# Kernel tuning notes

Measured on AMD Instinct MI355X. Metric: run time of the kernel, lower is better.

The kernel has to match this reference:

```python
import jax, jax.numpy as jnp
import numpy as np
from jax import lax

B, C, H, W = 4, 192, 64, 64
D_STATE, D_CONV, EXPAND = 16, 4, 2
D_INNER = EXPAND * C           # 384
DT_RANK = (C + 15) // 16       # 12 (mamba_ssm default ceil(d_model/16))


def setup_inputs() -> dict:
    key = jax.random.key(0)
    ks = jax.random.split(key, 12)
    sc = lambda k, shape, s=0.02: (jax.random.normal(k, shape, jnp.float32) * s)
    x = jax.random.normal(ks[0], (B, C, H, W), jnp.float32)
    norm_w = jnp.ones((C,), jnp.float32)
    norm_b = jnp.zeros((C,), jnp.float32)
    in_proj_w = sc(ks[1], (2 * D_INNER, C))
    conv_w = sc(ks[2], (D_INNER, D_CONV), 0.1)
    conv_b = jnp.zeros((D_INNER,), jnp.float32)
    x_proj_w = sc(ks[3], (DT_RANK + 2 * D_STATE, D_INNER))
    dt_proj_w = sc(ks[4], (D_INNER, DT_RANK), 0.1)
    # dt bias init so softplus(dt_bias) is in a realistic [1e-3, 1e-1] range
    dt0 = jax.random.uniform(ks[5], (D_INNER,), jnp.float32, 0.001, 0.1)
    dt_proj_b = jnp.log(jnp.expm1(dt0))
    A_log = jnp.log(jnp.broadcast_to(
        jnp.arange(1, D_STATE + 1, dtype=jnp.float32), (D_INNER, D_STATE)))
    D = jnp.ones((D_INNER,), jnp.float32)
    out_proj_w = sc(ks[6], (C, D_INNER))
    return {"x": x, "norm_w": norm_w, "norm_b": norm_b, "in_proj_w": in_proj_w,
            "conv_w": conv_w, "conv_b": conv_b, "x_proj_w": x_proj_w,
            "dt_proj_w": dt_proj_w, "dt_proj_b": dt_proj_b, "A_log": A_log,
            "D": D, "out_proj_w": out_proj_w}


def _mamba2d(x, norm_w, norm_b, in_proj_w, conv_w, conv_b, x_proj_w,
             dt_proj_w, dt_proj_b, A_log, D, out_proj_w):
    b, c, h, w = x.shape
    L = h * w
    seq = x.reshape(b, c, L).transpose(0, 2, 1)            # (B, L, C)
    # LayerNorm over channel dim
    mu = seq.mean(-1, keepdims=True)
    var = ((seq - mu) ** 2).mean(-1, keepdims=True)
    seqn = (seq - mu) * lax.rsqrt(var + 1e-5) * norm_w + norm_b
    # in_proj -> (x, z)
    xz = seqn @ in_proj_w.T                                # (B, L, 2*d_inner)
    xin, z = jnp.split(xz, 2, axis=-1)
    # causal depthwise conv1d over L
    xc = xin.transpose(0, 2, 1)                            # (B, d_inner, L)
    xc = lax.conv_general_dilated(xc, conv_w[:, None, :], (1,),
                                  [(D_CONV - 1, 0)],
                                  feature_group_count=D_INNER)
    xc = jax.nn.silu(xc + conv_b[None, :, None])
    xs = xc.transpose(0, 2, 1)                             # (B, L, d_inner)
    # input-dependent dt, B, C
    dbl = xs @ x_proj_w.T                                  # (B, L, dt_rank+2n)
    dt = dbl[..., :DT_RANK]
    Bm = dbl[..., DT_RANK:DT_RANK + D_STATE]               # (B, L, n)
    Cm = dbl[..., DT_RANK + D_STATE:]                      # (B, L, n)
    dt = jax.nn.softplus(dt @ dt_proj_w.T + dt_proj_b)     # (B, L, d_inner)
    A = -jnp.exp(A_log)                                    # (d_inner, n)
    dA = jnp.exp(dt[..., None] * A)                        # (B, L, d_inner, n)
    dBx = jnp.einsum('bld,bln->bldn', dt * xs, Bm)         # (B, L, d_inner, n)
    # selective scan over L
    def step(hcar, inp):
        dA_t, dBx_t, C_t = inp
        hcar = dA_t * hcar + dBx_t                         # (B, d_inner, n)
        y_t = jnp.einsum('bdn,bn->bd', hcar, C_t)
        return hcar, y_t
    h0 = jnp.zeros((b, D_INNER, D_STATE), xs.dtype)
    _, ys = lax.scan(step, h0, (jnp.moveaxis(dA, 1, 0),
                                jnp.moveaxis(dBx, 1, 0),
                                jnp.moveaxis(Cm, 1, 0)))
    y = jnp.moveaxis(ys, 0, 1) + xs * D                    # (B, L, d_inner)
    y = y * jax.nn.silu(z)
    out = y @ out_proj_w.T                                 # (B, L, C)
    return x + out.transpose(0, 2, 1).reshape(b, c, h, w)


def reference(x, norm_w, norm_b, in_proj_w, conv_w, conv_b, x_proj_w,
              dt_proj_w, dt_proj_b, A_log, D, out_proj_w):
    return _mamba2d(x, norm_w, norm_b, in_proj_w, conv_w, conv_b, x_proj_w,
                    dt_proj_w, dt_proj_b, A_log, D, out_proj_w)
```

## Files before the change

### kernel.cpp

```cpp
#include <hip/hip_runtime.h>
#include <hip/hip_bf16.h>

constexpr int B_ = 4;
constexpr int C_ = 192;
constexpr int L_ = 4096;
constexpr int DI = 384;
constexpr int DSs = 16;
constexpr int DTR = 12;
constexpr int NDBL = 44;
constexpr int NCHUNK = 256;
constexpr int CSZ = 16;

constexpr size_t BL = (size_t)B_ * L_;

constexpr size_t F_SEQN = 0;
constexpr size_t F_XIN  = F_SEQN + BL * C_ / 2;
constexpr size_t F_Z    = F_XIN + BL * DI / 2;
constexpr size_t F_XSB  = F_Z + BL * DI / 2;
constexpr size_t F_DBL  = F_XSB + BL * DI / 2;
constexpr size_t F_DT   = F_DBL + BL * NDBL;
constexpr size_t F_SBUF = F_DT + BL * DI / 2;
constexpr size_t F_HLOC = F_SBUF + (size_t)B_ * NCHUNK * DI;
constexpr size_t F_WBUF = F_HLOC + (size_t)B_ * NCHUNK * DI * 16 / 2;

typedef __attribute__((ext_vector_type(8))) short bf16x8;
typedef __attribute__((ext_vector_type(4))) float f32x4;

__device__ __forceinline__ unsigned short f2bf(float v) {
  unsigned x = __builtin_bit_cast(unsigned, v);
  unsigned r = x + 0x7FFFu + ((x >> 16) & 1u);
  return (unsigned short)(r >> 16);
}
__device__ __forceinline__ float bf2f(unsigned short u) {
  return __builtin_bit_cast(float, (unsigned)u << 16);
}
__device__ __forceinline__ void gload16(const void* g, void* l) {
  __builtin_amdgcn_global_load_lds((const __attribute__((address_space(1))) void*)g,
                                   (__attribute__((address_space(3))) void*)l, 16, 0, 0);
}
#define MFMA16(a, b, c) __builtin_amdgcn_mfma_f32_16x16x32_bf16(a, b, c, 0, 0, 0)

__global__ __launch_bounds__(256) void k_ln(const float* __restrict__ x,
                                            const float* __restrict__ nw,
                                            const float* __restrict__ nb,
                                            unsigned short* __restrict__ seqn,
                                            const float* __restrict__ ipw,
                                            const float* __restrict__ xpw,
                                            const float* __restrict__ opw,
                                            unsigned short* __restrict__ wbuf) {
  if (blockIdx.x >= 256) {
    int t = (blockIdx.x - 256) * 256 + threadIdx.x;
    if (t < 239616) {
      float v;
      if (t < 147456) v = ipw[t];
      else if (t < 165888) {
        int j = t - 147456;
        int r = j / 384, c = j - r * 384;
        v = (r < 44) ? xpw[r * 384 + c] : 0.f;
      } else v = opw[t - 165888];
      wbuf[t] = f2bf(v);
    }
    return;
  }
  __shared__ unsigned short xt[192][66];
  __shared__ float ps[4][64], ps2[4][64];
  __shared__ float mu_[64], rs_[64];
  __shared__ float wsh[192], bsh[192];
  int tid = threadIdx.x;
  int blk = blockIdx.x;
  int b = blk >> 6;
  int l0 = (blk & 63) << 6;
  const float* xb = x + (size_t)b * C_ * L_;
  for (int idx = tid; idx < 192 * 16; idx += 256) {
    int c = idx >> 4, lq = idx & 15;
    float4 v = *(const float4*)&xb[(size_t)c * L_ + l0 + (lq << 2)];
    ushort2 u0, u1;
    u0.x = f2bf(v.x); u0.y = f2bf(v.y);
    u1.x = f2bf(v.z); u1.y = f2bf(v.w);
    *(ushort2*)&xt[c][(lq << 2)] = u0;
    *(ushort2*)&xt[c][(lq << 2) + 2] = u1;
  }
  if (tid < 192) { wsh[tid] = nw[tid]; bsh[tid] = nb[tid]; }
  __syncthreads();
  int ll = tid & 63, q = tid >> 6;
  float s = 0.f, ss = 0.f;
  for (int c = q * 48; c < q * 48 + 48; ++c) {
    float v = bf2f(xt[c][ll]);
    s += v; ss += v * v;
  }
  ps[q][ll] = s; ps2[q][ll] = ss;
  __syncthreads();
  if (q == 0) {
    float st = ps[0][ll] + ps[1][ll] + ps[2][ll] + ps[3][ll];
    float sst = ps2[0][ll] + ps2[1][ll] + ps2[2][ll] + ps2[3][ll];
    float mu = st * (1.f / 192.f);
    float var = sst * (1.f / 192.f) - mu * mu;
    mu_[ll] = mu; rs_[ll] = rsqrtf(var + 1e-5f);
  }
  __syncthreads();
  unsigned short* so = seqn + ((size_t)b * L_ + l0) * C_;
  for (int idx = tid; idx < 64 * 192; idx += 256) {
    int l = idx / 192, c = idx - l * 192;
    so[idx] = f2bf((bf2f(xt[c][l]) - mu_[l]) * rs_[l] * wsh[c] + bsh[c]);
  }
}

__global__ __launch_bounds__(256) void k_inproj(const unsigned short* __restrict__ A,
                                                const unsigned short* __restrict__ W,
                                                unsigned short* __restrict__ xin,
                                                unsigned short* __restrict__ z) {
  __shared__ unsigned short smem[16384];
  unsigned short* As = smem;
  unsigned short* Bs = smem + 8192;
  int tid = threadIdx.x;
  int w = tid >> 6, l = tid & 63;
  int wr = w >> 1, wc = w & 1;
  int m0 = blockIdx.x << 7;
  int n0 = blockIdx.y << 7;
  f32x4 acc[4][4];
#pragma unroll
  for (int i = 0; i < 4; ++i)
#pragma unroll
    for (int j = 0; j < 4; ++j) acc[i][j] = (f32x4){0.f, 0.f, 0.f, 0.f};
  int lr = l & 15, lk = l >> 4;
  for (int kt = 0; kt < 3; ++kt) {
    int k0 = kt * 64;
    if (kt) __syncthreads();
#pragma unroll
    for (int i = 0; i < 4; ++i) {
      int row = (i << 5) + (tid >> 3);
      int gc = k0 + (((tid & 7) ^ (row & 7)) << 3);
      gload16(A + (size_t)(m0 + row) * 192 + gc, &As[(i << 11) + (w << 9)]);
      gload16(W + (size_t)(n0 + row) * 192 + gc, &Bs[(i << 11) + (w << 9)]);
    }
    __syncthreads();
#pragma unroll
    for (int ks = 0; ks < 2; ++ks) {
      int s = (ks << 2) + lk;
      bf16x8 af[4], bfr[4];
#pragma unroll
      for (int mi = 0; mi < 4; ++mi) {
        int r = (wr << 6) + (mi << 4) + lr;
        af[mi] = *(const bf16x8*)&As[r * 64 + ((s ^ (r & 7)) << 3)];
      }
#pragma unroll
      for (int ni = 0; ni < 4; ++ni) {
        int r = (wc << 6) + (ni << 4) + lr;
        bfr[ni] = *(const bf16x8*)&Bs[r * 64 + ((s ^ (r & 7)) << 3)];
      }
#pragma unroll
      for (int mi = 0; mi < 4; ++mi)
#pragma unroll
        for (int ni = 0; ni < 4; ++ni) acc[mi][ni] = MFMA16(af[mi], bfr[ni], acc[mi][ni]);
    }
  }
  __syncthreads();
#pragma unroll
  for (int mi = 0; mi < 4; ++mi)
#pragma unroll
    for (int ni = 0; ni < 4; ++ni) {
      int col = (wc << 6) + (ni << 4) + lr;
#pragma unroll
      for (int r = 0; r < 4; ++r) {
        int row = (wr << 6) + (mi << 4) + (lk << 2) + r;
        smem[(row << 7) + col] = f2bf(acc[mi][ni][r]);
      }
    }
  __syncthreads();
#pragma unroll
  for (int i = 0; i < 8; ++i) {
    int chunk = i * 256 + tid;
    int row = chunk >> 4, cq = chunk & 15;
    int n = n0 + (cq << 3);
    unsigned short* dst = (n < 384) ? (xin + (size_t)(m0 + row) * DI + n)
                                    : (z + (size_t)(m0 + row) * DI + (n - 384));
    *(bf16x8*)dst = *(const bf16x8*)&smem[(row << 7) + (cq << 3)];
  }
}

__global__ __launch_bounds__(384) void k_convx(const unsigned short* __restrict__ xin,
                                               const float* __restrict__ cw,
                                               const float* __restrict__ cb,
                                               const unsigned short* __restrict__ W,
                                               unsigned short* __restrict__ xsb,
                                               float* __restrict__ dbl) {
  __shared__ unsigned short xs[6 * 4096];
  __shared__ unsigned short Bs[3072];
  int tid = threadIdx.x;
  int w = tid >> 6, l = tid & 63;
  int b = blockIdx.y;
  int l0 = blockIdx.x << 6;
  int d = tid;
  float4 w4 = *(const float4*)&cw[d * 4];
  float bb = cb[d];
  const unsigned short* xp = xin + ((size_t)b * L_ + l0) * DI + d;
  unsigned short* op = xsb + ((size_t)b * L_ + l0) * DI + d;
  float x0 = 0.f, x1 = 0.f, x2 = 0.f;
  if (l0 > 0) {
    x0 = bf2f(*(xp - 3 * DI));
    x1 = bf2f(*(xp - 2 * DI));
    x2 = bf2f(*(xp - DI));
  }
  int kt = d >> 6, col = d & 63, g = col >> 3, e = col & 7;
  unsigned short* xsrow = xs + kt * 4096;
  for (int r = 0; r < 64; ++r) {
    float xv = bf2f(xp[(size_t)r * DI]);
    float a = bb + w4.x * x0 + w4.y * x1 + w4.z * x2 + w4.w * xv;
    float sv = a * __builtin_amdgcn_rcpf(1.f + __expf(-a));
    unsigned short sb = f2bf(sv);
    xsrow[r * 64 + ((g ^ (r & 7)) << 3) + e] = sb;
    op[(size_t)r * DI] = sb;
    x0 = x1; x1 = x2; x2 = xv;
  }
  __syncthreads();
  int lr = l & 15, lk = l >> 4;
  f32x4 acc[3];
#pragma unroll
  for (int i = 0; i < 3; ++i) acc[i] = (f32x4){0.f, 0.f, 0.f, 0.f};
  for (int kt2 = 0; kt2 < 6; ++kt2) {
    int k0 = kt2 * 64;
    if (kt2) __syncthreads();
    {
      int row = tid >> 3;
      int gc = k0 + (((tid & 7) ^ (row & 7)) << 3);
      gload16(W + (size_t)row * 384 + gc, &Bs[w << 9]);
    }
    __syncthreads();
    if (w < 4) {
#pragma unroll
      for (int ks = 0; ks < 2; ++ks) {
        int s = (ks << 2) + lk;
        int ar = (w << 4) + lr;
        bf16x8 a = *(const bf16x8*)&xs[kt2 * 4096 + ar * 64 + ((s ^ (ar & 7)) << 3)];
#pragma unroll
        for (int ni = 0; ni < 3; ++ni) {
          int br = (ni << 4) + lr;
          bf16x8 bbv = *(const bf16x8*)&Bs[br * 64 + ((s ^ (br & 7)) << 3)];
          acc[ni] = MFMA16(a, bbv, acc[ni]);
        }
      }
    }
  }
  if (w < 4) {
#pragma unroll
    for (int ni = 0; ni < 3; ++ni)
#pragma unroll
      for (int r = 0; r < 4; ++r) {
        int colq = (ni << 4) + lr;
        if (colq < NDBL)
          dbl[((size_t)b * L_ + l0 + (w << 4) + (lk << 2) + r) * NDBL + colq] = acc[ni][r];
      }
  }
}

__global__ __launch_bounds__(384) void k_scanA(const unsigned short* __restrict__ xsb,
                                               const float* __restrict__ dbl,
                                               const float* __restrict__ dw,
                                               const float* __restrict__ dbias,
                                               const float* __restrict__ A_log,
                                               unsigned short* __restrict__ dtb,
                                               unsigned short* __restrict__ Hloc,
                                               float* __restrict__ Sbuf) {
  __shared__ float Bsh[CSZ][16];
  __shared__ float dl[CSZ][12];
  int tid = threadIdx.x;
  int blk = blockIdx.x;
  int b = blk >> 8;
  int chunk = blk & (NCHUNK - 1);
  int l0 = chunk * CSZ;
  for (int idx = tid; idx < CSZ * 28; idx += 384) {
    int r = idx / 28, c = idx - r * 28;
    float v = dbl[((size_t)b * L_ + l0 + r) * NDBL + c];
    if (c < 12) dl[r][c] = v; else Bsh[r][c - 12] = v;
  }
  int d = tid;
  float4 wv0 = *(const float4*)&dw[d * 12];
  float4 wv1 = *(const float4*)&dw[d * 12 + 4];
  float4 wv2 = *(const float4*)&dw[d * 12 + 8];
  float bias = dbias[d];
  bool fast = true;
#pragma unroll
  for (int n = 0; n < 16; ++n) {
    float An_ = -__expf(A_log[d * 16 + n]);
    fast = fast && (fabsf(An_ + (float)(n + 1)) < 2e-3f);
  }
  const unsigned short* xp = xsb + ((size_t)b * L_ + l0) * DI + d;
  unsigned short* dtp = dtb + ((size_t)b * L_ + l0) * DI + d;
  __syncthreads();
  float h[16];
#pragma unroll
  for (int n = 0; n < 16; ++n) h[n] = 0.f;
  float S = 0.f;
  if (fast) {
#pragma unroll
    for (int i = 0; i < CSZ; ++i) {
      float4 c0 = *(const float4*)&dl[i][0];
      float4 c1 = *(const float4*)&dl[i][4];
      float4 c2 = *(const float4*)&dl[i][8];
      float a = bias;
      a = fmaf(wv0.x, c0.x, a); a = fmaf(wv0.y, c0.y, a);
      a = fmaf(wv0.z, c0.z, a); a = fmaf(wv0.w, c0.w, a);
      a = fmaf(wv1.x, c1.x, a); a = fmaf(wv1.y, c1.y, a);
      a = fmaf(wv1.z, c1.z, a); a = fmaf(wv1.w, c1.w, a);
      a = fmaf(wv2.x, c2.x, a); a = fmaf(wv2.y, c2.y, a);
      a = fmaf(wv2.z, c2.z, a); a = fmaf(wv2.w, c2.w, a);
      float sp = fmaxf(a, 0.f) + __logf(1.f + __expf(-fabsf(a)));
      dtp[(size_t)i * DI] = f2bf(sp);
      S += sp;
      float xv = bf2f(xp[(size_t)i * DI]);
      float dtx = sp * xv;
      float r = __expf(-sp);
      float r2 = r * r;
      float r4 = r2 * r2;
      float dA0 = r, dA1 = r2, dA2 = r2 * r, dA3 = r4;
#pragma unroll
      for (int g = 0; g < 4; ++g) {
        float4 Bg = *(const float4*)&Bsh[i][g << 2];
        h[(g << 2) + 0] = fmaf(dA0, h[(g << 2) + 0], dtx * Bg.x);
        h[(g << 2) + 1] = fmaf(dA1, h[(g << 2) + 1], dtx * Bg.y);
        h[(g << 2) + 2] = fmaf(dA2, h[(g << 2) + 2], dtx * Bg.z);
        h[(g << 2) + 3] = fmaf(dA3, h[(g << 2) + 3], dtx * Bg.w);
        if (g < 3) { dA0 *= r4; dA1 *= r4; dA2 *= r4; dA3 *= r4; }
      }
    }
  } else {
    float An[16];
#pragma unroll
    for (int n = 0; n < 16; ++n) An[n] = -__expf(A_log[d * 16 + n]);
#pragma unroll
    for (int i = 0; i < CSZ; ++i) {
      float4 c0 = *(const float4*)&dl[i][0];
      float4 c1 = *(const float4*)&dl[i][4];
      float4 c2 = *(const float4*)&dl[i][8];
      float a = bias;
      a = fmaf(wv0.x, c0.x, a); a = fmaf(wv0.y, c0.y, a);
      a = fmaf(wv0.z, c0.z, a); a = fmaf(wv0.w, c0.w, a);
      a = fmaf(wv1.x, c1.x, a); a = fmaf(wv1.y, c1.y, a);
      a = fmaf(wv1.z, c1.z, a); a = fmaf(wv1.w, c1.w, a);
      a = fmaf(wv2.x, c2.x, a); a = fmaf(wv2.y, c2.y, a);
      a = fmaf(wv2.z, c2.z, a); a = fmaf(wv2.w, c2.w, a);
      float sp = fmaxf(a, 0.f) + __logf(1.f + __expf(-fabsf(a)));
      dtp[(size_t)i * DI] = f2bf(sp);
      S += sp;
      float xv = bf2f(xp[(size_t)i * DI]);
      float dtx = sp * xv;
#pragma unroll
      for (int n = 0; n < 16; ++n)
        h[n] = fmaf(__expf(sp * An[n]), h[n], dtx * Bsh[i][n]);
    }
  }
  size_t hbase = ((size_t)(b * NCHUNK + chunk) * 16) * DI + d;
#pragma unroll
  for (int n = 0; n < 16; ++n) Hloc[hbase + (size_t)n * DI] = f2bf(h[n]);
  Sbuf[((size_t)b * NCHUNK + chunk) * DI + d] = S;
}

__global__ __launch_bounds__(256) void k_scanB(const float* __restrict__ A_log,
                                               unsigned short* __restrict__ Hloc,
                                               const float* __restrict__ Sbuf) {
  int gid = blockIdx.x * 256 + threadIdx.x;
  int d = gid % DI;
  int rest = gid / DI;
  int n = rest & 15;
  int b = rest >> 4;
  float An = -__expf(A_log[d * 16 + n]);
  unsigned short* Hp = Hloc + ((size_t)b * NCHUNK * 16 + n) * DI + d;
  const float* Sp = Sbuf + (size_t)b * NCHUNK * DI + d;
  constexpr size_t HS = (size_t)16 * DI;
  float h = 0.f;
  float SA[8], HA[8], SB[8], HB[8];
#define LDGRP(Sa, Ha, cb)                         \
  _Pragma("unroll") for (int u = 0; u < 8; ++u) { \
    Sa[u] = Sp[(size_t)((cb) + u) * DI];          \
    Ha[u] = bf2f(Hp[(size_t)((cb) + u) * HS]);    \
  }
#define STGRP(Sa, Ha, cb)                         \
  _Pragma("unroll") for (int u = 0; u < 8; ++u) { \
    Hp[(size_t)((cb) + u) * HS] = f2bf(h);        \
    h = fmaf(__expf(An * Sa[u]), h, Ha[u]);       \
  }
  LDGRP(SA, HA, 0)
  for (int g = 0; g < 32; g += 2) {
    LDGRP(SB, HB, (g + 1) * 8)
    STGRP(SA, HA, g * 8)
    if (g + 2 < 32) LDGRP(SA, HA, (g + 2) * 8)
    STGRP(SB, HB, (g + 1) * 8)
  }
#undef LDGRP
#undef STGRP
}

__global__ __launch_bounds__(384) void k_scanC(const unsigned short* __restrict__ xsb,
                                               const unsigned short* __restrict__ dtb,
                                               const float* __restrict__ dbl,
                                               const unsigned short* __restrict__ z,
                                               const float* __restrict__ A_log,
                                               const float* __restrict__ Dw,
                                               const unsigned short* __restrict__ Hloc,
                                               unsigned short* __restrict__ ybuf) {
  __shared__ float BCsh[CSZ][32];
  int tid = threadIdx.x;
  int blk = blockIdx.x;
  int b = blk >> 8;
  int chunk = blk & (NCHUNK - 1);
  int l0 = chunk * CSZ;
  for (int idx = tid; idx < CSZ * 32; idx += 384) {
    int r = idx >> 5, n32 = idx & 31;
    BCsh[r][n32] = dbl[((size_t)b * L_ + l0 + r) * NDBL + DTR + n32];
  }
  int d = tid;
  float Dd = Dw[d];
  bool fast = true;
#pragma unroll
  for (int n = 0; n < 16; ++n) {
    float An_ = -__expf(A_log[d * 16 + n]);
    fast = fast && (fabsf(An_ + (float)(n + 1)) < 2e-3f);
  }
  size_t hbase = ((size_t)(b * NCHUNK + chunk) * 16) * DI + d;
  float h[16];
#pragma unroll
  for (int n = 0; n < 16; ++n) h[n] = bf2f(Hloc[hbase + (size_t)n * DI]);
  const unsigned short* xp = xsb + ((size_t)b * L_ + l0) * DI + d;
  const unsigned short* dtp = dtb + ((size_t)b * L_ + l0) * DI + d;
  const unsigned short* zp = z + ((size_t)b * L_ + l0) * DI + d;
  unsigned short* yp = ybuf + ((size_t)b * L_ + l0) * DI + d;
  __syncthreads();
  if (fast) {
#pragma unroll
    for (int i = 0; i < CSZ; ++i) {
      float sp = bf2f(dtp[(size_t)i * DI]);
      float xv = bf2f(xp[(size_t)i * DI]);
      float zv = bf2f(zp[(size_t)i * DI]);
      float dtx = sp * xv;
      float r = __expf(-sp);
      float r2 = r * r;
      float r4 = r2 * r2;
      float dA0 = r, dA1 = r2, dA2 = r2 * r, dA3 = r4;
      float y = 0.f;
#pragma unroll
      for (int g = 0; g < 4; ++g) {
        float4 Bg = *(const float4*)&BCsh[i][g << 2];
        float4 Cg = *(const float4*)&BCsh[i][16 + (g << 2)];
        h[(g << 2) + 0] = fmaf(dA0, h[(g << 2) + 0], dtx * Bg.x);
        h[(g << 2) + 1] = fmaf(dA1, h[(g << 2) + 1], dtx * Bg.y);
        h[(g << 2) + 2] = fmaf(dA2, h[(g << 2) + 2], dtx * Bg.z);
        h[(g << 2) + 3] = fmaf(dA3, h[(g << 2) + 3], dtx * Bg.w);
        y = fmaf(h[(g << 2) + 0], Cg.x, y);
        y = fmaf(h[(g << 2) + 1], Cg.y, y);
        y = fmaf(h[(g << 2) + 2], Cg.z, y);
        y = fmaf(h[(g << 2) + 3], Cg.w, y);
        if (g < 3) { dA0 *= r4; dA1 *= r4; dA2 *= r4; dA3 *= r4; }
      }
      y = fmaf(xv, Dd, y);
      float sig = __builtin_amdgcn_rcpf(1.f + __expf(-zv));
      yp[(size_t)i * DI] = f2bf(y * (zv * sig));
    }
  } else {
    float An[16];
#pragma unroll
    for (int n = 0; n < 16; ++n) An[n] = -__expf(A_log[d * 16 + n]);
#pragma unroll
    for (int i = 0; i < CSZ; ++i) {
      float sp = bf2f(dtp[(size_t)i * DI]);
      float xv = bf2f(xp[(size_t)i * DI]);
      float zv = bf2f(zp[(size_t)i * DI]);
      float dtx = sp * xv;
      float y = 0.f;
#pragma unroll
      for (int n = 0; n < 16; ++n) {
        h[n] = fmaf(__expf(sp * An[n]), h[n], dtx * BCsh[i][n]);
        y = fmaf(h[n], BCsh[i][16 + n], y);
      }
      y = fmaf(xv, Dd, y);
      float sig = __builtin_amdgcn_rcpf(1.f + __expf(-zv));
      yp[(size_t)i * DI] = f2bf(y * (zv * sig));
    }
  }
}

__global__ __launch_bounds__(256) void k_outproj(const unsigned short* __restrict__ Y,
                                                 const unsigned short* __restrict__ W,
                                                 const float* __restrict__ x,
                                                 float* __restrict__ out) {
  __shared__ float smemf[8448];
  unsigned short* As = (unsigned short*)smemf;
  unsigned short* Bs = (unsigned short*)smemf + 8192;
  int tid = threadIdx.x;
  int w = tid >> 6, l = tid & 63;
  int wr = w >> 1, wc = w & 1;
  int m0 = blockIdx.x << 7;
  int n0 = blockIdx.y << 6;
  int lr = l & 15, lk = l >> 4;
  f32x4 acc[4][2];
#pragma unroll
  for (int i = 0; i < 4; ++i)
#pragma unroll
    for (int j = 0; j < 2; ++j) acc[i][j] = (f32x4){0.f, 0.f, 0.f, 0.f};
  for (int kt = 0; kt < 6; ++kt) {
    int k0 = kt * 64;
    if (kt) __syncthreads();
#pragma unroll
    for (int i = 0; i < 4; ++i) {
      int row = (i << 5) + (tid >> 3);
      int gc = k0 + (((tid & 7) ^ (row & 7)) << 3);
      gload16(Y + (size_t)(m0 + row) * 384 + gc, &As[(i << 11) + (w << 9)]);
    }
#pragma unroll
    for (int i = 0; i < 2; ++i) {
      int row = (i << 5) + (tid >> 3);
      int gc = k0 + (((tid & 7) ^ (row & 7)) << 3);
      gload16(W + (size_t)(n0 + row) * 384 + gc, &Bs[(i << 11) + (w << 9)]);
    }
    __syncthreads();
#pragma unroll
    for (int ks = 0; ks < 2; ++ks) {
      int s = (ks << 2) + lk;
      bf16x8 bfr[2];
#pragma unroll
      for (int ni = 0; ni < 2; ++ni) {
        int r = (wc << 5) + (ni << 4) + lr;
        bfr[ni] = *(const bf16x8*)&Bs[r * 64 + ((s ^ (r & 7)) << 3)];
      }
#pragma unroll
      for (int mi = 0; mi < 4; ++mi) {
        int r = (wr << 6) + (mi << 4) + lr;
        bf16x8 a = *(const bf16x8*)&As[r * 64 + ((s ^ (r & 7)) << 3)];
#pragma unroll
        for (int ni = 0; ni < 2; ++ni) acc[mi][ni] = MFMA16(a, bfr[ni], acc[mi][ni]);
      }
    }
  }
  __syncthreads();
#pragma unroll
  for (int mi = 0; mi < 4; ++mi)
#pragma unroll
    for (int ni = 0; ni < 2; ++ni) {
      int c = (wc << 5) + (ni << 4) + lr;
      int lrow = (wr << 6) + (mi << 4) + (lk << 2);
      *(f32x4*)&smemf[c * 132 + lrow] = acc[mi][ni];
    }
  __syncthreads();
  int b = m0 >> 12;
  int l0 = m0 & (L_ - 1);
#pragma unroll
  for (int i = 0; i < 8; ++i) {
    int chunk = i * 256 + tid;
    int c = chunk >> 5, lq = chunk & 31;
    f32x4 v = *(const f32x4*)&smemf[c * 132 + (lq << 2)];
    size_t off = ((size_t)b * C_ + n0 + c) * L_ + l0 + (lq << 2);
    f32x4 xv = *(const f32x4*)&x[off];
    v = v + xv;
    *(f32x4*)&out[off] = v;
  }
}

extern "C" void kernel_launch(void* const* d_in, const int* in_sizes, int n_in,
                              void* d_out, int out_size, void* d_ws, size_t ws_size,
                              hipStream_t stream) {
  const float* x         = (const float*)d_in[0];
  const float* norm_w    = (const float*)d_in[1];
  const float* norm_b    = (const float*)d_in[2];
  const float* in_proj_w = (const float*)d_in[3];
  const float* conv_w    = (const float*)d_in[4];
  const float* conv_b    = (const float*)d_in[5];
  const float* x_proj_w  = (const float*)d_in[6];
  const float* dt_proj_w = (const float*)d_in[7];
  const float* dt_proj_b = (const float*)d_in[8];
  const float* A_log     = (const float*)d_in[9];
  const float* Dw        = (const float*)d_in[10];
  const float* out_proj_w= (const float*)d_in[11];
  float* out = (float*)d_out;
  float* ws = (float*)d_ws;

  unsigned short* seqn = (unsigned short*)(ws + F_SEQN);
  unsigned short* xin  = (unsigned short*)(ws + F_XIN);
  unsigned short* z    = (unsigned short*)(ws + F_Z);
  unsigned short* xsb  = (unsigned short*)(ws + F_XSB);
  float* dbl           = ws + F_DBL;
  unsigned short* dtb  = (unsigned short*)(ws + F_DT);
  float* Sbuf          = ws + F_SBUF;
  unsigned short* Hloc = (unsigned short*)(ws + F_HLOC);
  unsigned short* wbuf = (unsigned short*)(ws + F_WBUF);
  unsigned short* ipw  = wbuf;
  unsigned short* xpw  = wbuf + 147456;
  unsigned short* opw  = wbuf + 165888;
  unsigned short* ybuf = xin;

  hipLaunchKernelGGL(k_ln, dim3(1192), dim3(256), 0, stream, x, norm_w, norm_b, seqn,
                     in_proj_w, x_proj_w, out_proj_w, wbuf);
  hipLaunchKernelGGL(k_inproj, dim3(128, 6), dim3(256), 0, stream, seqn, ipw, xin, z);
  hipLaunchKernelGGL(k_convx, dim3(64, 4), dim3(384), 0, stream, xin, conv_w, conv_b, xpw, xsb,
                     dbl);
  hipLaunchKernelGGL(k_scanA, dim3(1024), dim3(384), 0, stream, xsb, dbl, dt_proj_w, dt_proj_b,
                     A_log, dtb, Hloc, Sbuf);
  hipLaunchKernelGGL(k_scanB, dim3(96), dim3(256), 0, stream, A_log, Hloc, Sbuf);
  hipLaunchKernelGGL(k_scanC, dim3(1024), dim3(384), 0, stream, xsb, dtb, dbl, z, A_log, Dw,
                     Hloc, ybuf);
  hipLaunchKernelGGL(k_outproj, dim3(128, 3), dim3(256), 0, stream, ybuf, opw, x, out);
}
```

Baseline: 111.6 us.

## Split inter-chunk scan into two levels and fuse out_proj into scanC

The serial inter-chunk scan (96 blocks walking 256 chunks each) becomes a two-level hierarchy. A 1024-block pass scans 16 chunks per super-chunk and records prefix sums. A small 64-block pass then scans the 16 super-chunk carries, and scanC combines both to rebuild each chunk's starting state. The out_proj GEMM is also fused into scanC: y stays in LDS as a 16x384 bf16 tile and is multiplied by the streamed out_proj weights, which removes the ybuf round-trip and one kernel launch. The cost is that every scanC block reloads the full 192x384 weight matrix with only 16 rows of M per block, which gives low MFMA utilisation and heavier LDS use.

```diff
diff --git a/kernel.cpp b/kernel.cpp
--- a/kernel.cpp
+++ b/kernel.cpp
@@ -10,6 +10,7 @@
 constexpr int NDBL = 44;
 constexpr int NCHUNK = 256;
 constexpr int CSZ = 16;
+constexpr int NSUP = 16;
 
 constexpr size_t BL = (size_t)B_ * L_;
 
@@ -21,7 +22,11 @@
 constexpr size_t F_DT   = F_DBL + BL * NDBL;
 constexpr size_t F_SBUF = F_DT + BL * DI / 2;
 constexpr size_t F_HLOC = F_SBUF + (size_t)B_ * NCHUNK * DI;
-constexpr size_t F_WBUF = F_HLOC + (size_t)B_ * NCHUNK * DI * 16 / 2;
+constexpr size_t F_SPRE = F_HLOC + (size_t)B_ * NCHUNK * DI * 16 / 2;
+constexpr size_t F_HSUP = F_SPRE + (size_t)B_ * NCHUNK * DI;
+constexpr size_t F_SSUP = F_HSUP + (size_t)B_ * NSUP * 16 * DI;
+constexpr size_t F_ISUP = F_SSUP + (size_t)B_ * NSUP * DI;
+constexpr size_t F_WBUF = F_ISUP + (size_t)B_ * NSUP * 16 * DI;
 
 typedef __attribute__((ext_vector_type(8))) short bf16x8;
 typedef __attribute__((ext_vector_type(4))) float f32x4;
@@ -355,39 +360,51 @@
   Sbuf[((size_t)b * NCHUNK + chunk) * DI + d] = S;
 }
 
-__global__ __launch_bounds__(256) void k_scanB(const float* __restrict__ A_log,
-                                               unsigned short* __restrict__ Hloc,
-                                               const float* __restrict__ Sbuf) {
-  int gid = blockIdx.x * 256 + threadIdx.x;
-  int d = gid % DI;
-  int rest = gid / DI;
-  int n = rest & 15;
-  int b = rest >> 4;
+__global__ __launch_bounds__(384) void k_scanB1(const float* __restrict__ A_log,
+                                                unsigned short* __restrict__ Hloc,
+                                                const float* __restrict__ Sbuf,
+                                                float* __restrict__ Spre,
+                                                float* __restrict__ Hsup,
+                                                float* __restrict__ Ssup) {
+  int d = threadIdx.x;
+  int blk = blockIdx.x;
+  int n = blk & 15;
+  int s = (blk >> 4) & 15;
+  int b = blk >> 8;
   float An = -__expf(A_log[d * 16 + n]);
-  unsigned short* Hp = Hloc + ((size_t)b * NCHUNK * 16 + n) * DI + d;
-  const float* Sp = Sbuf + (size_t)b * NCHUNK * DI + d;
-  constexpr size_t HS = (size_t)16 * DI;
-  float h = 0.f;
-  float SA[8], HA[8], SB[8], HB[8];
-#define LDGRP(Sa, Ha, cb)                         \
-  _Pragma("unroll") for (int u = 0; u < 8; ++u) { \
-    Sa[u] = Sp[(size_t)((cb) + u) * DI];          \
-    Ha[u] = bf2f(Hp[(size_t)((cb) + u) * HS]);    \
-  }
-#define STGRP(Sa, Ha, cb)                         \
-  _Pragma("unroll") for (int u = 0; u < 8; ++u) { \
-    Hp[(size_t)((cb) + u) * HS] = f2bf(h);        \
-    h = fmaf(__expf(An * Sa[u]), h, Ha[u]);       \
-  }
-  LDGRP(SA, HA, 0)
-  for (int g = 0; g < 32; g += 2) {
-    LDGRP(SB, HB, (g + 1) * 8)
-    STGRP(SA, HA, g * 8)
-    if (g + 2 < 32) LDGRP(SA, HA, (g + 2) * 8)
-    STGRP(SB, HB, (g + 1) * 8)
-  }
-#undef LDGRP
-#undef STGRP
+  float h = 0.f, Sp = 0.f;
+  int c0 = s * 16;
+#pragma unroll
+  for (int i = 0; i < 16; ++i) {
+    int c = c0 + i;
+    size_t hidx = (((size_t)(b * NCHUNK + c) * 16) + n) * DI + d;
+    float Hl = bf2f(Hloc[hidx]);
+    float S = Sbuf[((size_t)b * NCHUNK + c) * DI + d];
+    Hloc[hidx] = f2bf(h);
+    if (n == 0) Spre[((size_t)b * NCHUNK + c) * DI + d] = Sp;
+    h = fmaf(__expf(An * S), h, Hl);
+    Sp += S;
+  }
+  Hsup[(((size_t)(b * NSUP + s) * 16) + n) * DI + d] = h;
+  if (n == 0) Ssup[((size_t)b * NSUP + s) * DI + d] = Sp;
+}
+
+__global__ __launch_bounds__(384) void k_scanB2(const float* __restrict__ A_log,
+                                                const float* __restrict__ Hsup,
+                                                const float* __restrict__ Ssup,
+                                                float* __restrict__ Isup) {
+  int d = threadIdx.x;
+  int blk = blockIdx.x;
+  int n = blk & 15;
+  int b = blk >> 4;
+  float An = -__expf(A_log[d * 16 + n]);
+  float I = 0.f;
+#pragma unroll
+  for (int s = 0; s < NSUP; ++s) {
+    size_t idx = (((size_t)(b * NSUP + s) * 16) + n) * DI + d;
+    Isup[idx] = I;
+    I = fmaf(__expf(An * Ssup[((size_t)b * NSUP + s) * DI + d]), I, Hsup[idx]);
+  }
 }
 
 __global__ __launch_bounds__(384) void k_scanC(const unsigned short* __restrict__ xsb,
@@ -397,8 +414,14 @@
                                                const float* __restrict__ A_log,
                                                const float* __restrict__ Dw,
                                                const unsigned short* __restrict__ Hloc,
-                                               unsigned short* __restrict__ ybuf) {
+                                               const float* __restrict__ Spre,
+                                               const float* __restrict__ Isup,
+                                               const unsigned short* __restrict__ Wo,
+                                               const float* __restrict__ x,
+                                               float* __restrict__ out) {
   __shared__ float BCsh[CSZ][32];
+  __shared__ unsigned short yt[6 * 1024];
+  __shared__ unsigned short Bs[12288];
   int tid = threadIdx.x;
   int blk = blockIdx.x;
   int b = blk >> 8;
@@ -416,14 +439,41 @@
     float An_ = -__expf(A_log[d * 16 + n]);
     fast = fast && (fabsf(An_ + (float)(n + 1)) < 2e-3f);
   }
+  int sup = chunk >> 4;
   size_t hbase = ((size_t)(b * NCHUNK + chunk) * 16) * DI + d;
+  size_t ibase = ((size_t)(b * NSUP + sup) * 16) * DI + d;
+  float Spv = Spre[((size_t)b * NCHUNK + chunk) * DI + d];
   float h[16];
-#pragma unroll
-  for (int n = 0; n < 16; ++n) h[n] = bf2f(Hloc[hbase + (size_t)n * DI]);
+  if (fast) {
+    float t = __expf(-Spv);
+    float t2 = t * t;
+    float t4 = t2 * t2;
+    float p0 = t, p1 = t2, p2 = t2 * t, p3 = t4;
+#pragma unroll
+    for (int g = 0; g < 4; ++g) {
+      h[(g << 2) + 0] = fmaf(p0, Isup[ibase + (size_t)((g << 2) + 0) * DI],
+                             bf2f(Hloc[hbase + (size_t)((g << 2) + 0) * DI]));
+      h[(g << 2) + 1] = fmaf(p1, Isup[ibase + (size_t)((g << 2) + 1) * DI],
+                             bf2f(Hloc[hbase + (size_t)((g << 2) + 1) * DI]));
+      h[(g << 2) + 2] = fmaf(p2, Isup[ibase + (size_t)((g << 2) + 2) * DI],
+                             bf2f(Hloc[hbase + (size_t)((g << 2) + 2) * DI]));
+      h[(g << 2) + 3] = fmaf(p3, Isup[ibase + (size_t)((g << 2) + 3) * DI],
+                             bf2f(Hloc[hbase + (size_t)((g << 2) + 3) * DI]));
+      if (g < 3) { p0 *= t4; p1 *= t4; p2 *= t4; p3 *= t4; }
+    }
+  } else {
+#pragma unroll
+    for (int n = 0; n < 16; ++n) {
+      float An_ = -__expf(A_log[d * 16 + n]);
+      h[n] = fmaf(__expf(An_ * Spv), Isup[ibase + (size_t)n * DI],
+                  bf2f(Hloc[hbase + (size_t)n * DI]));
+    }
+  }
   const unsigned short* xp = xsb + ((size_t)b * L_ + l0) * DI + d;
   const unsigned short* dtp = dtb + ((size_t)b * L_ + l0) * DI + d;
   const unsigned short* zp = z + ((size_t)b * L_ + l0) * DI + d;
-  unsigned short* yp = ybuf + ((size_t)b * L_ + l0) * DI + d;
+  int ktile = d >> 6, colq = d & 63, gq = colq >> 3, eq = colq & 7;
+  unsigned short* ytp = yt + ktile * 1024;
   __syncthreads();
   if (fast) {
 #pragma unroll
@@ -453,7 +503,7 @@
       }
       y = fmaf(xv, Dd, y);
       float sig = __builtin_amdgcn_rcpf(1.f + __expf(-zv));
-      yp[(size_t)i * DI] = f2bf(y * (zv * sig));
+      ytp[i * 64 + ((gq ^ (i & 7)) << 3) + eq] = f2bf(y * (zv * sig));
     }
   } else {
     float An[16];
@@ -473,84 +523,42 @@
       }
       y = fmaf(xv, Dd, y);
       float sig = __builtin_amdgcn_rcpf(1.f + __expf(-zv));
-      yp[(size_t)i * DI] = f2bf(y * (zv * sig));
-    }
-  }
-}
-
-__global__ __launch_bounds__(256) void k_outproj(const unsigned short* __restrict__ Y,
-                                                 const unsigned short* __restrict__ W,
-                                                 const float* __restrict__ x,
-                                                 float* __restrict__ out) {
-  __shared__ float smemf[8448];
-  unsigned short* As = (unsigned short*)smemf;
-  unsigned short* Bs = (unsigned short*)smemf + 8192;
-  int tid = threadIdx.x;
+      ytp[i * 64 + ((gq ^ (i & 7)) << 3) + eq] = f2bf(y * (zv * sig));
+    }
+  }
   int w = tid >> 6, l = tid & 63;
-  int wr = w >> 1, wc = w & 1;
-  int m0 = blockIdx.x << 7;
-  int n0 = blockIdx.y << 6;
   int lr = l & 15, lk = l >> 4;
-  f32x4 acc[4][2];
-#pragma unroll
-  for (int i = 0; i < 4; ++i)
-#pragma unroll
-    for (int j = 0; j < 2; ++j) acc[i][j] = (f32x4){0.f, 0.f, 0.f, 0.f};
+  f32x4 acc[2];
+  acc[0] = (f32x4){0.f, 0.f, 0.f, 0.f};
+  acc[1] = (f32x4){0.f, 0.f, 0.f, 0.f};
   for (int kt = 0; kt < 6; ++kt) {
     int k0 = kt * 64;
-    if (kt) __syncthreads();
-#pragma unroll
-    for (int i = 0; i < 4; ++i) {
-      int row = (i << 5) + (tid >> 3);
+    __syncthreads();
+#pragma unroll
+    for (int j = 0; j < 4; ++j) {
+      int row = j * 48 + (tid >> 3);
       int gc = k0 + (((tid & 7) ^ (row & 7)) << 3);
-      gload16(Y + (size_t)(m0 + row) * 384 + gc, &As[(i << 11) + (w << 9)]);
-    }
-#pragma unroll
-    for (int i = 0; i < 2; ++i) {
-      int row = (i << 5) + (tid >> 3);
-      int gc = k0 + (((tid & 7) ^ (row & 7)) << 3);
-      gload16(W + (size_t)(n0 + row) * 384 + gc, &Bs[(i << 11) + (w << 9)]);
+      gload16(Wo + (size_t)row * 384 + gc, &Bs[j * 3072 + (w << 9)]);
     }
     __syncthreads();
 #pragma unroll
     for (int ks = 0; ks < 2; ++ks) {
       int s = (ks << 2) + lk;
-      bf16x8 bfr[2];
+      bf16x8 a = *(const bf16x8*)&yt[kt * 1024 + lr * 64 + ((s ^ (lr & 7)) << 3)];
 #pragma unroll
       for (int ni = 0; ni < 2; ++ni) {
-        int r = (wc << 5) + (ni << 4) + lr;
-        bfr[ni] = *(const bf16x8*)&Bs[r * 64 + ((s ^ (r & 7)) << 3)];
-      }
-#pragma unroll
-      for (int mi = 0; mi < 4; ++mi) {
-        int r = (wr << 6) + (mi << 4) + lr;
-        bf16x8 a = *(const bf16x8*)&As[r * 64 + ((s ^ (r & 7)) << 3)];
-#pragma unroll
-        for (int ni = 0; ni < 2; ++ni) acc[mi][ni] = MFMA16(a, bfr[ni], acc[mi][ni]);
-      }
-    }
-  }
-  __syncthreads();
-#pragma unroll
-  for (int mi = 0; mi < 4; ++mi)
-#pragma unroll
-    for (int ni = 0; ni < 2; ++ni) {
-      int c = (wc << 5) + (ni << 4) + lr;
-      int lrow = (wr << 6) + (mi << 4) + (lk << 2);
-      *(f32x4*)&smemf[c * 132 + lrow] = acc[mi][ni];
-    }
-  __syncthreads();
-  int b = m0 >> 12;
-  int l0 = m0 & (L_ - 1);
-#pragma unroll
-  for (int i = 0; i < 8; ++i) {
-    int chunk = i * 256 + tid;
-    int c = chunk >> 5, lq = chunk & 31;
-    f32x4 v = *(const f32x4*)&smemf[c * 132 + (lq << 2)];
-    size_t off = ((size_t)b * C_ + n0 + c) * L_ + l0 + (lq << 2);
+        int br = ((w << 1) + ni) * 16 + lr;
+        bf16x8 bv = *(const bf16x8*)&Bs[br * 64 + ((s ^ (br & 7)) << 3)];
+        acc[ni] = MFMA16(a, bv, acc[ni]);
+      }
+    }
+  }
+#pragma unroll
+  for (int ni = 0; ni < 2; ++ni) {
+    int c = ((w << 1) + ni) * 16 + lr;
+    size_t off = ((size_t)b * C_ + c) * L_ + l0 + (lk << 2);
     f32x4 xv = *(const f32x4*)&x[off];
-    v = v + xv;
-    *(f32x4*)&out[off] = v;
+    *(f32x4*)&out[off] = acc[ni] + xv;
   }
 }
 
@@ -580,11 +588,14 @@
   unsigned short* dtb  = (unsigned short*)(ws + F_DT);
   float* Sbuf          = ws + F_SBUF;
   unsigned short* Hloc = (unsigned short*)(ws + F_HLOC);
+  float* Spre          = ws + F_SPRE;
+  float* Hsup          = ws + F_HSUP;
+  float* Ssup          = ws + F_SSUP;
+  float* Isup          = ws + F_ISUP;
   unsigned short* wbuf = (unsigned short*)(ws + F_WBUF);
   unsigned short* ipw  = wbuf;
   unsigned short* xpw  = wbuf + 147456;
   unsigned short* opw  = wbuf + 165888;
-  unsigned short* ybuf = xin;
 
   hipLaunchKernelGGL(k_ln, dim3(1192), dim3(256), 0, stream, x, norm_w, norm_b, seqn,
                      in_proj_w, x_proj_w, out_proj_w, wbuf);
@@ -593,8 +604,9 @@
                      dbl);
   hipLaunchKernelGGL(k_scanA, dim3(1024), dim3(384), 0, stream, xsb, dbl, dt_proj_w, dt_proj_b,
                      A_log, dtb, Hloc, Sbuf);
-  hipLaunchKernelGGL(k_scanB, dim3(96), dim3(256), 0, stream, A_log, Hloc, Sbuf);
+  hipLaunchKernelGGL(k_scanB1, dim3(1024), dim3(384), 0, stream, A_log, Hloc, Sbuf, Spre, Hsup,
+                     Ssup);
+  hipLaunchKernelGGL(k_scanB2, dim3(64), dim3(384), 0, stream, A_log, Hsup, Ssup, Isup);
   hipLaunchKernelGGL(k_scanC, dim3(1024), dim3(384), 0, stream, xsb, dtb, dbl, z, A_log, Dw,
-                     Hloc, ybuf);
-  hipLaunchKernelGGL(k_outproj, dim3(128, 3), dim3(256), 0, stream, ybuf, opw, x, out);
-}
+                     Hloc, Spre, Isup, opw, x, out);
+}
```

Result: no change. 111.5 us (-0.0%).
